# Kernel optimization log

Hardware: AMD Instinct MI355X
Metric: run time of the kernel (lower is better)

Reference implementation:

```python
import jax, jax.numpy as jnp
import numpy as np

D = 1024        # d_model
H = 16          # query heads
HKV = 4         # kv heads (GQA)
HD = D // H     # head dim = 64
MAX_T = 1024
EPS = 1e-6
CAP = 50.0      # logit softcap


def _rope_cache(max_t, hd):
    inv = 1.0 / (10000.0 ** (np.arange(0, hd, 2, dtype=np.float32) / hd))  # (hd/2,)
    t = np.arange(max_t, dtype=np.float32)
    f = np.outer(t, inv)                                                   # (max_t, hd/2)
    return jnp.asarray(np.cos(f)), jnp.asarray(np.sin(f))


def setup_inputs() -> dict:
    key = jax.random.key(0)
    ks = jax.random.split(key, 5)
    x = jax.random.normal(ks[0], (2, 64, 256, D), jnp.float32)  # (B,T,S,D)
    wq = jax.random.normal(ks[1], (D, H * HD), jnp.float32) * 0.02
    wk = jax.random.normal(ks[2], (D, HKV * HD), jnp.float32) * 0.02
    wv = jax.random.normal(ks[3], (D, HKV * HD), jnp.float32) * 0.02
    wo = jax.random.normal(ks[4], (H * HD, D), jnp.float32) * 0.02
    q_scale = jnp.ones((HD,), jnp.float32)  # QKNorm learnable gains
    k_scale = jnp.ones((HD,), jnp.float32)
    rope_cos, rope_sin = _rope_cache(MAX_T, HD)
    return {"x": x, "wq": wq, "wk": wk, "wv": wv, "wo": wo,
            "q_scale": q_scale, "k_scale": k_scale,
            "rope_cos": rope_cos, "rope_sin": rope_sin}


def _rmsnorm(v, scale):
    return v * jax.lax.rsqrt(jnp.mean(v * v, axis=-1, keepdims=True) + EPS) * scale


def reference(x, wq, wk, wv, wo, q_scale, k_scale, rope_cos, rope_sin):
    B, T, S, Dm = x.shape
    # fold spatial positions into batch: each position attends causally over time
    xt = x.transpose(0, 2, 1, 3).reshape(B * S, T, Dm)          # (N,T,D)
    q = (xt @ wq).reshape(B * S, T, H, HD)
    k = (xt @ wk).reshape(B * S, T, HKV, HD)
    v = (xt @ wv).reshape(B * S, T, HKV, HD)
    # QK-norm (RMSNorm over head_dim) before RoPE
    q = _rmsnorm(q, q_scale)
    k = _rmsnorm(k, k_scale)
    # 1D RoPE over temporal positions (split-half convention)
    cos = rope_cos[:T][None, :, None, :]                        # (1,T,1,HD/2)
    sin = rope_sin[:T][None, :, None, :]

    def rot(u):
        u1, u2 = jnp.split(u, 2, axis=-1)
        return jnp.concatenate([u1 * cos - u2 * sin, u1 * sin + u2 * cos], axis=-1)

    q = rot(q)
    k = rot(k)
    # GQA: expand kv heads to match query heads
    rep = H // HKV
    k = jnp.repeat(k, rep, axis=2)
    v = jnp.repeat(v, rep, axis=2)
    scores = jnp.einsum('nthd,nshd->nhts', q, k) / np.float32(np.sqrt(HD))
    scores = CAP * jnp.tanh(scores / CAP)                        # logit softcap
    causal = jnp.tril(jnp.ones((T, T), bool))
    scores = jnp.where(causal, scores, jnp.float32(-1e30))
    a = jax.nn.softmax(scores, axis=-1)
    o = jnp.einsum('nhts,nshd->nthd', a, v).reshape(B * S, T, H * HD) @ wo
    return o.reshape(B, S, T, Dm).transpose(0, 2, 1, 3)          # (B,T,S,D)
```

## Files before the change

kernel.cpp:

```cpp
#include <hip/hip_runtime.h>
#include <hip/hip_bf16.h>

#define DM   1024
#define NHQ  16
#define NKVH 4
#define HDIM 64
#define TTT  64
#define SSS  256
#define NBB  2
#define MROWS 32768

using short8 = __attribute__((ext_vector_type(8))) short;
using short4v = __attribute__((ext_vector_type(4))) short;
using f32x4  = __attribute__((ext_vector_type(4))) float;

__device__ __forceinline__ short f2bf(float f) {
  union { __hip_bfloat16 h; short s; } u;
  u.h = __float2bfloat16(f);
  return u.s;
}

__device__ __forceinline__ f32x4 mfma16(short8 a, short8 b, f32x4 c) {
  return __builtin_amdgcn_mfma_f32_16x16x32_bf16(a, b, c, 0, 0, 0);
}

__device__ __forceinline__ void gload_lds16(const void* g, void* l) {
  __builtin_amdgcn_global_load_lds(
      (const __attribute__((address_space(1))) void*)g,
      (__attribute__((address_space(3))) void*)l, 16, 0, 0);
}

__global__ __launch_bounds__(256) void k_prep(const float* __restrict__ x,
                                              short* __restrict__ xb,
                                              const float* __restrict__ wq,
                                              const float* __restrict__ wk,
                                              const float* __restrict__ wv,
                                              const float* __restrict__ wo,
                                              short* __restrict__ wqkvT,
                                              short* __restrict__ woT) {
  __shared__ float tile[32][33];
  int bid = blockIdx.x;
  if (bid < 4096) {
    float4 v[8];
    #pragma unroll
    for (int i = 0; i < 8; ++i) {
      int r = bid * 8 + i;
      int n = r >> 6, t = r & 63;
      int b = n >> 8, s = n & 255;
      v[i] = ((const float4*)(x + ((size_t)((b * TTT + t) * SSS + s)) * DM))[threadIdx.x];
    }
    #pragma unroll
    for (int i = 0; i < 8; ++i) {
      int r = bid * 8 + i;
      short4 o;
      o.x = f2bf(v[i].x); o.y = f2bf(v[i].y); o.z = f2bf(v[i].z); o.w = f2bf(v[i].w);
      ((short4*)(xb + (size_t)r * DM))[threadIdx.x] = o;
    }
    return;
  }
  bid -= 4096;
  const float* w; short* wt; int cols;
  if (bid < 1024)      { w = wq; wt = wqkvT; cols = 1024; }
  else if (bid < 1280) { w = wk; wt = wqkvT + (size_t)1024 * 1024; cols = 256; bid -= 1024; }
  else if (bid < 1536) { w = wv; wt = wqkvT + (size_t)1280 * 1024; cols = 256; bid -= 1280; }
  else                 { w = wo; wt = woT; cols = 1024; bid -= 1536; }
  int ctiles = cols >> 5;
  int tj = bid % ctiles;
  int td = bid / ctiles;
  int lx = threadIdx.x & 31, ly = threadIdx.x >> 5;
  #pragma unroll
  for (int rr = 0; rr < 32; rr += 8)
    tile[rr + ly][lx] = w[(size_t)(td * 32 + rr + ly) * cols + tj * 32 + lx];
  __syncthreads();
  #pragma unroll
  for (int rr = 0; rr < 32; rr += 8)
    wt[(size_t)(tj * 32 + rr + ly) * 1024 + td * 32 + lx] = f2bf(tile[lx][rr + ly]);
}

#define TILE(RAK0, RAK1, RBK0, RBK1, NLB, CLB, G, IA, IB, VM)                  \
  {                                                                            \
    short8 a[4], b0[4], b1[4];                                                 \
    _Pragma("unroll") for (int n = 0; n < 4; ++n)                              \
        b0[n] = *(const short8*)(RBK0 + n * 1024);                             \
    _Pragma("unroll") for (int m = 0; m < 4; ++m)                              \
        a[m] = *(const short8*)(RAK0 + m * 1024);                              \
    if (IA) stA0(NLB, (G + 1) * 64);                                           \
    __builtin_amdgcn_s_barrier();                                              \
    asm volatile("s_waitcnt lgkmcnt(0)" ::: "memory");                         \
    __builtin_amdgcn_s_setprio(1);                                             \
    _Pragma("unroll") for (int m = 0; m < 4; ++m)                              \
      _Pragma("unroll") for (int n = 0; n < 4; ++n)                            \
          acc[m][n] = mfma16(a[m], b0[n], acc[m][n]);                          \
    __builtin_amdgcn_s_setprio(0);                                             \
    __builtin_amdgcn_s_barrier();                                              \
    _Pragma("unroll") for (int m = 0; m < 4; ++m)                              \
        a[m] = *(const short8*)(RAK0 + 4096 + m * 1024);                       \
    if (IA) stA1(NLB, (G + 1) * 64);                                           \
    __builtin_amdgcn_s_barrier();                                              \
    asm volatile("s_waitcnt lgkmcnt(0)" ::: "memory");                         \
    __builtin_amdgcn_s_setprio(1);                                             \
    _Pragma("unroll") for (int m = 0; m < 4; ++m)                              \
      _Pragma("unroll") for (int n = 0; n < 4; ++n)                            \
          acc[4 + m][n] = mfma16(a[m], b0[n], acc[4 + m][n]);                  \
    __builtin_amdgcn_s_setprio(0);                                             \
    __builtin_amdgcn_s_barrier();                                              \
    _Pragma("unroll") for (int n = 0; n < 4; ++n)                              \
        b1[n] = *(const short8*)(RBK1 + n * 1024);                             \
    _Pragma("unroll") for (int m = 0; m < 4; ++m)                              \
        a[m] = *(const short8*)(RAK1 + m * 1024);                              \
    __builtin_amdgcn_s_barrier();                                              \
    asm volatile("s_waitcnt lgkmcnt(0)" ::: "memory");                         \
    __builtin_amdgcn_s_setprio(1);                                             \
    _Pragma("unroll") for (int m = 0; m < 4; ++m)                              \
      _Pragma("unroll") for (int n = 0; n < 4; ++n)                            \
          acc[m][n] = mfma16(a[m], b1[n], acc[m][n]);                          \
    __builtin_amdgcn_s_setprio(0);                                             \
    __builtin_amdgcn_s_barrier();                                              \
    _Pragma("unroll") for (int m = 0; m < 4; ++m)                              \
        a[m] = *(const short8*)(RAK1 + 4096 + m * 1024);                       \
    if (IB) stB(CLB, (G + 2) * 64);                                            \
    __builtin_amdgcn_s_barrier();                                              \
    asm volatile("s_waitcnt lgkmcnt(0)" ::: "memory");                         \
    __builtin_amdgcn_s_setprio(1);                                             \
    _Pragma("unroll") for (int m = 0; m < 4; ++m)                              \
      _Pragma("unroll") for (int n = 0; n < 4; ++n)                            \
          acc[4 + m][n] = mfma16(a[m], b1[n], acc[4 + m][n]);                  \
    __builtin_amdgcn_s_setprio(0);                                             \
    if (VM == 4)      asm volatile("s_waitcnt vmcnt(4)" ::: "memory");         \
    else if (VM == 0) asm volatile("s_waitcnt vmcnt(0)" ::: "memory");         \
    __builtin_amdgcn_s_barrier();                                              \
  }

__device__ __forceinline__ void gemm256(const short* __restrict__ Ab,
                                        const short* __restrict__ Bb,
                                        short* __restrict__ sm,
                                        f32x4 (&acc)[8][4]) {
  const int tid = threadIdx.x, lane = tid & 63, wid = tid >> 6;
  const int wr = wid >> 2, wc = wid & 3;
  const int ln15 = lane & 15, lhi = lane >> 4;
  const int rsw = ln15 & 7;
  const int row_t = tid >> 3;
  const int sw = ((tid & 7) ^ (row_t & 7)) << 3;
  const short* pA0 = Ab + (size_t)row_t * 1024 + sw;
  const short* pA1 = pA0 + (size_t)64 * 1024;
  const short* pA2 = pA0 + (size_t)128 * 1024;
  const short* pA3 = pA0 + (size_t)192 * 1024;
  const short* pB0 = Bb + (size_t)row_t * 1024 + sw;
  const short* pB1 = pB0 + (size_t)64 * 1024;
  const short* pB2 = pB0 + (size_t)128 * 1024;
  const short* pB3 = pB0 + (size_t)192 * 1024;
  auto stA0 = [&](short* lb, int kt) {
    gload_lds16(pA0 + kt, lb + tid * 8);
    gload_lds16(pA1 + kt, lb + 4096 + tid * 8);
  };
  auto stA1 = [&](short* lb, int kt) {
    gload_lds16(pA2 + kt, lb + 8192 + tid * 8);
    gload_lds16(pA3 + kt, lb + 12288 + tid * 8);
  };
  auto stB = [&](short* lb, int kt) {
    gload_lds16(pB0 + kt, lb + 16384 + tid * 8);
    gload_lds16(pB1 + kt, lb + 20480 + tid * 8);
    gload_lds16(pB2 + kt, lb + 24576 + tid * 8);
    gload_lds16(pB3 + kt, lb + 28672 + tid * 8);
  };
  const int sk0 = (lhi ^ rsw) << 3;
  const int sk1 = ((4 + lhi) ^ rsw) << 3;
  const short* rA0k0 = sm + (wr * 128 + ln15) * 64 + sk0;
  const short* rA0k1 = sm + (wr * 128 + ln15) * 64 + sk1;
  const short* rB0k0 = sm + 16384 + (wc * 64 + ln15) * 64 + sk0;
  const short* rB0k1 = sm + 16384 + (wc * 64 + ln15) * 64 + sk1;
  const short* rA1k0 = rA0k0 + 32768;
  const short* rA1k1 = rA0k1 + 32768;
  const short* rB1k0 = rB0k0 + 32768;
  const short* rB1k1 = rB0k1 + 32768;
  short* buf0 = sm;
  short* buf1 = sm + 32768;
  stA0(buf0, 0); stA1(buf0, 0); stB(buf0, 0);
  stA0(buf1, 64); stA1(buf1, 64); stB(buf1, 64);
  asm volatile("s_waitcnt vmcnt(8)" ::: "memory");
  __builtin_amdgcn_s_barrier();
  TILE(rA0k0, rA0k1, rB0k0, rB0k1, buf1, buf0, 0, 0, 1, 4)
  TILE(rA1k0, rA1k1, rB1k0, rB1k1, buf0, buf1, 1, 1, 1, 4)
  for (int gg = 1; gg < 7; ++gg) {
    const int g0 = gg * 2;
    TILE(rA0k0, rA0k1, rB0k0, rB0k1, buf1, buf0, g0, 1, 1, 4)
    TILE(rA1k0, rA1k1, rB1k0, rB1k1, buf0, buf1, g0 + 1, 1, 1, 4)
  }
  TILE(rA0k0, rA0k1, rB0k0, rB0k1, buf1, buf0, 14, 1, 0, 0)
  TILE(rA1k0, rA1k1, rB1k0, rB1k1, buf0, buf1, 15, 0, 0, -1)
}

__global__ __launch_bounds__(512) void k_qkv(
    const short* __restrict__ xb, const short* __restrict__ wt,
    const float* __restrict__ qscale, const float* __restrict__ kscale,
    const float* __restrict__ rcos, const float* __restrict__ rsin,
    short* __restrict__ qb, short* __restrict__ kb, short* __restrict__ vb) {
  __shared__ __align__(16) short sm[65536];
  const int bid = blockIdx.x;
  const int swz = (bid & 7) * 96 + (bid >> 3);
  const int tn = swz % 6, tm = swz / 6;
  f32x4 acc[8][4] = {};
  gemm256(xb + (size_t)tm * 256 * 1024, wt + (size_t)tn * 256 * 1024, sm, acc);

  const int tid = threadIdx.x, lane = tid & 63, wid = tid >> 6;
  const int wr = wid >> 2, wc = wid & 3;
  const int ln15 = lane & 15, lhi = lane >> 4;
  short* ot = sm;
  if (tn < 5) {
    const float* scale = (tn < 4) ? qscale : kscale;
    float sc[4];
    #pragma unroll
    for (int n = 0; n < 4; ++n) sc[n] = scale[n * 16 + ln15];
    #pragma unroll
    for (int m = 0; m < 8; ++m) {
      #pragma unroll
      for (int j = 0; j < 4; ++j) {
        float ss = 0.f;
        #pragma unroll
        for (int n = 0; n < 4; ++n) { float v = acc[m][n][j]; ss += v * v; }
        #pragma unroll
        for (int off = 8; off; off >>= 1) ss += __shfl_xor(ss, off, 64);
        float rms = rsqrtf(ss * (1.f / 64.f) + 1e-6f);
        int rl = wr * 128 + m * 16 + lhi * 4 + j;
        int t = (tm * 256 + rl) & 63;
        #pragma unroll
        for (int n = 0; n < 2; ++n) {
          int i = n * 16 + ln15;
          float cs = rcos[t * 32 + i], sn = rsin[t * 32 + i];
          float v1 = acc[m][n][j] * rms * sc[n];
          float v2 = acc[m][n + 2][j] * rms * sc[n + 2];
          ot[rl * 256 + wc * 64 + i]      = f2bf(v1 * cs - v2 * sn);
          ot[rl * 256 + wc * 64 + i + 32] = f2bf(v1 * sn + v2 * cs);
        }
      }
    }
  } else {
    #pragma unroll
    for (int m = 0; m < 8; ++m)
      #pragma unroll
      for (int n = 0; n < 4; ++n)
        #pragma unroll
        for (int j = 0; j < 4; ++j) {
          int rl = wr * 128 + m * 16 + lhi * 4 + j;
          ot[rl * 256 + wc * 64 + n * 16 + ln15] = f2bf(acc[m][n][j]);
        }
  }
  __syncthreads();
  {
    int row = tid >> 1, half = tid & 1;
    int r = tm * 256 + row;
    const uint4* src = (const uint4*)(ot + row * 256 + half * 128);
    short* dst;
    if (tn < 4)       dst = qb + (size_t)r * 1024 + tn * 256 + half * 128;
    else if (tn == 4) dst = kb + (size_t)r * 256 + half * 128;
    else              dst = vb + (size_t)r * 256 + half * 128;
    uint4* d4 = (uint4*)dst;
    #pragma unroll
    for (int i = 0; i < 16; ++i) d4[i] = src[i];
  }
}

__global__ __launch_bounds__(512) void k_attn(const short* __restrict__ qb,
                                              const short* __restrict__ kb,
                                              const short* __restrict__ vb,
                                              short* __restrict__ ob) {
  __shared__ __align__(16) short Vt[256 * 72];
  __shared__ __align__(16) short Ps[8][64 * 72];
  const int n = blockIdx.x;
  const int tid = threadIdx.x, lane = tid & 63, wid = tid >> 6;
  const int ln15 = lane & 15, lhi = lane >> 4;
  {
    const short* vrow = vb + ((size_t)(n * 64 + lane)) * 256;
    #pragma unroll
    for (int i = 0; i < 4; ++i) {
      int d = wid * 32 + i * 8;
      short8 vv = *(const short8*)(vrow + d);
      #pragma unroll
      for (int e = 0; e < 8; ++e) Vt[(d + e) * 72 + lane] = vv[e];
    }
  }
  short8 aq[2][4][2];
  #pragma unroll
  for (int hh = 0; hh < 2; ++hh)
    #pragma unroll
    for (int nn = 0; nn < 4; ++nn)
      #pragma unroll
      for (int kk = 0; kk < 2; ++kk)
        aq[hh][nn][kk] = *(const short8*)(qb + ((size_t)(n * 64 + nn * 16 + ln15)) * 1024
                                             + (wid + hh * 8) * 64 + kk * 32 + lhi * 8);
  __syncthreads();
  short* Pt = &Ps[wid][0];
  #pragma unroll
  for (int hh = 0; hh < 2; ++hh) {
    const int h = wid + hh * 8;
    const int kvh = h >> 2;
    short8 bk[4][2];
    #pragma unroll
    for (int m = 0; m < 4; ++m)
      #pragma unroll
      for (int kk = 0; kk < 2; ++kk)
        bk[m][kk] = *(const short8*)(kb + ((size_t)(n * 64 + m * 16 + ln15)) * 256
                                        + kvh * 64 + kk * 32 + lhi * 8);
    f32x4 sa[4][4] = {};
    __builtin_amdgcn_s_setprio(1);
    #pragma unroll
    for (int kk = 0; kk < 2; ++kk)
      #pragma unroll
      for (int m = 0; m < 4; ++m)
        #pragma unroll
        for (int nn = 0; nn < 4; ++nn)
          sa[m][nn] = mfma16(bk[m][kk], aq[hh][nn][kk], sa[m][nn]);
    __builtin_amdgcn_s_setprio(0);
    #pragma unroll
    for (int m = 0; m < 4; ++m)
      #pragma unroll
      for (int nn = 0; nn < 4; ++nn)
        #pragma unroll
        for (int j = 0; j < 4; ++j) {
          float e2 = __expf(sa[m][nn][j] * 0.005f);
          float cap = 50.f * (e2 - 1.f) * __builtin_amdgcn_rcpf(e2 + 1.f);
          int scur = m * 16 + lhi * 4 + j, tcur = nn * 16 + ln15;
          sa[m][nn][j] = (scur <= tcur) ? cap : -1e30f;
        }
    float inv[4];
    #pragma unroll
    for (int nn = 0; nn < 4; ++nn) {
      float mx = -3e38f;
      #pragma unroll
      for (int m = 0; m < 4; ++m)
        #pragma unroll
        for (int j = 0; j < 4; ++j) mx = fmaxf(mx, sa[m][nn][j]);
      mx = fmaxf(mx, __shfl_xor(mx, 16, 64));
      mx = fmaxf(mx, __shfl_xor(mx, 32, 64));
      float sum = 0.f;
      #pragma unroll
      for (int m = 0; m < 4; ++m)
        #pragma unroll
        for (int j = 0; j < 4; ++j) {
          float e = __expf(sa[m][nn][j] - mx);
          sa[m][nn][j] = e; sum += e;
        }
      sum += __shfl_xor(sum, 16, 64);
      sum += __shfl_xor(sum, 32, 64);
      inv[nn] = __builtin_amdgcn_rcpf(sum);
    }
    #pragma unroll
    for (int nn = 0; nn < 4; ++nn)
      #pragma unroll
      for (int m = 0; m < 4; ++m) {
        short4v w;
        #pragma unroll
        for (int j = 0; j < 4; ++j) w[j] = f2bf(sa[m][nn][j] * inv[nn]);
        *(short4v*)(Pt + (nn * 16 + ln15) * 72 + m * 16 + lhi * 4) = w;
      }
    short8 ap[4][2], bv[4][2];
    #pragma unroll
    for (int m = 0; m < 4; ++m)
      #pragma unroll
      for (int kk = 0; kk < 2; ++kk)
        ap[m][kk] = *(const short8*)(Pt + (m * 16 + ln15) * 72 + kk * 32 + lhi * 8);
    #pragma unroll
    for (int nn = 0; nn < 4; ++nn)
      #pragma unroll
      for (int kk = 0; kk < 2; ++kk)
        bv[nn][kk] = *(const short8*)(&Vt[(kvh * 64 + nn * 16 + ln15) * 72 + kk * 32 + lhi * 8]);
    f32x4 oa[4][4] = {};
    __builtin_amdgcn_s_setprio(1);
    #pragma unroll
    for (int kk = 0; kk < 2; ++kk)
      #pragma unroll
      for (int m = 0; m < 4; ++m)
        #pragma unroll
        for (int nn = 0; nn < 4; ++nn)
          oa[m][nn] = mfma16(ap[m][kk], bv[nn][kk], oa[m][nn]);
    __builtin_amdgcn_s_setprio(0);
    #pragma unroll
    for (int m = 0; m < 4; ++m)
      #pragma unroll
      for (int nn = 0; nn < 4; ++nn)
        #pragma unroll
        for (int j = 0; j < 4; ++j)
          Pt[(m * 16 + lhi * 4 + j) * 72 + nn * 16 + ln15] = f2bf(oa[m][nn][j]);
    #pragma unroll
    for (int c = 0; c < 8; ++c)
      *(uint4*)(ob + ((size_t)(n * 64 + lane)) * 1024 + h * 64 + c * 8)
          = *(const uint4*)(Pt + lane * 72 + c * 8);
  }
}

__global__ __launch_bounds__(512) void k_out(const short* __restrict__ ab,
                                             const short* __restrict__ wt,
                                             float* __restrict__ out) {
  __shared__ __align__(16) short sm[65536];
  const int bid = blockIdx.x;
  const int swz = (bid & 7) * 64 + (bid >> 3);
  const int tn = swz & 3, tm = swz >> 2;
  f32x4 acc[8][4] = {};
  gemm256(ab + (size_t)tm * 256 * 1024, wt + (size_t)tn * 256 * 1024, sm, acc);

  const int tid = threadIdx.x, lane = tid & 63, wid = tid >> 6;
  const int wr = wid >> 2, wc = wid & 3;
  const int ln15 = lane & 15, lhi = lane >> 4;
  float* of = (float*)sm;
  #pragma unroll
  for (int ch = 0; ch < 2; ++ch) {
    if (wr == ch) {
      #pragma unroll
      for (int m = 0; m < 8; ++m)
        #pragma unroll
        for (int n = 0; n < 4; ++n)
          #pragma unroll
          for (int j = 0; j < 4; ++j)
            of[(m * 16 + lhi * 4 + j) * 256 + wc * 64 + n * 16 + ln15] = acc[m][n][j];
    }
    __syncthreads();
    {
      int row = tid >> 2, q4 = tid & 3;
      int r = tm * 256 + ch * 128 + row;
      int nseq = r >> 6, t = r & 63;
      int b = nseq >> 8, s = nseq & 255;
      float* dst = out + ((size_t)((b * TTT + t) * SSS + s)) * DM + tn * 256 + q4 * 64;
      const float4* src = (const float4*)(of + row * 256 + q4 * 64);
      float4* d4 = (float4*)dst;
      #pragma unroll
      for (int i = 0; i < 16; ++i) d4[i] = src[i];
    }
    __syncthreads();
  }
}

extern "C" void kernel_launch(void* const* d_in, const int* in_sizes, int n_in,
                              void* d_out, int out_size, void* d_ws, size_t ws_size,
                              hipStream_t stream) {
  const float* x  = (const float*)d_in[0];
  const float* wq = (const float*)d_in[1];
  const float* wk = (const float*)d_in[2];
  const float* wv = (const float*)d_in[3];
  const float* wo = (const float*)d_in[4];
  const float* qs = (const float*)d_in[5];
  const float* ks = (const float*)d_in[6];
  const float* rc = (const float*)d_in[7];
  const float* rs = (const float*)d_in[8];
  float* out = (float*)d_out;
  char* ws = (char*)d_ws;

  short* xb    = (short*)(ws);
  short* wqkvT = (short*)(ws + 67108864);
  short* woT   = (short*)(ws + 70254592);
  short* qb    = (short*)(ws + 72351744);
  short* kb    = (short*)(ws + 139460608);
  short* vb    = (short*)(ws + 156237824);
  short* ob    = xb;

  k_prep<<<6656, 256, 0, stream>>>(x, xb, wq, wk, wv, wo, wqkvT, woT);
  k_qkv<<<768, 512, 0, stream>>>(xb, wqkvT, qs, ks, rc, rs, qb, kb, vb);
  k_attn<<<512, 512, 0, stream>>>(qb, kb, vb, ob);
  k_out<<<512, 512, 0, stream>>>(ob, woT, out);
}
```

Before: 323.0 us.

## Process two sequences per attention block with double-buffered V prefetch

Each attention block now handles two consecutive (batch*spatial) sequences instead of one, and the grid is halved. V rows for both sequences are loaded into registers up front, with the second sequence's V written to a second LDS buffer while the first is processed. This aims to hide global load latency and amortize block launch cost. The trade-off is more LDS per block and more register pressure, which may lower occupancy, and with 256 blocks some CUs may sit idle.

Measured after the change: 318.8 us (median of 2 runs). Within noise of the previous version (-1.3%).

```diff
diff --git a/kernel.cpp b/kernel.cpp
--- a/kernel.cpp
+++ b/kernel.cpp
@@ -264,127 +264,145 @@
                                               const short* __restrict__ kb,
                                               const short* __restrict__ vb,
                                               short* __restrict__ ob) {
-  __shared__ __align__(16) short Vt[256 * 72];
+  __shared__ __align__(16) short Vt[2][256 * 72];
   __shared__ __align__(16) short Ps[8][64 * 72];
-  const int n = blockIdx.x;
+  const int n0 = blockIdx.x * 2;
   const int tid = threadIdx.x, lane = tid & 63, wid = tid >> 6;
   const int ln15 = lane & 15, lhi = lane >> 4;
+  short8 vr0[4], vr1[4];
   {
-    const short* vrow = vb + ((size_t)(n * 64 + lane)) * 256;
-    #pragma unroll
-    for (int i = 0; i < 4; ++i) {
-      int d = wid * 32 + i * 8;
-      short8 vv = *(const short8*)(vrow + d);
-      #pragma unroll
-      for (int e = 0; e < 8; ++e) Vt[(d + e) * 72 + lane] = vv[e];
-    }
-  }
-  short8 aq[2][4][2];
+    const short* vrow0 = vb + ((size_t)(n0 * 64 + lane)) * 256;
+    const short* vrow1 = vrow0 + 64 * 256;
+    #pragma unroll
+    for (int i = 0; i < 4; ++i) vr1[i] = *(const short8*)(vrow1 + wid * 32 + i * 8);
+    #pragma unroll
+    for (int i = 0; i < 4; ++i) vr0[i] = *(const short8*)(vrow0 + wid * 32 + i * 8);
+  }
   #pragma unroll
-  for (int hh = 0; hh < 2; ++hh)
-    #pragma unroll
-    for (int nn = 0; nn < 4; ++nn)
-      #pragma unroll
-      for (int kk = 0; kk < 2; ++kk)
-        aq[hh][nn][kk] = *(const short8*)(qb + ((size_t)(n * 64 + nn * 16 + ln15)) * 1024
-                                             + (wid + hh * 8) * 64 + kk * 32 + lhi * 8);
-  __syncthreads();
+  for (int i = 0; i < 4; ++i) {
+    int d = wid * 32 + i * 8;
+    #pragma unroll
+    for (int e = 0; e < 8; ++e) Vt[0][(d + e) * 72 + lane] = vr0[i][e];
+  }
   short* Pt = &Ps[wid][0];
   #pragma unroll
-  for (int hh = 0; hh < 2; ++hh) {
-    const int h = wid + hh * 8;
-    const int kvh = h >> 2;
-    short8 bk[4][2];
-    #pragma unroll
-    for (int m = 0; m < 4; ++m)
+  for (int ss = 0; ss < 2; ++ss) {
+    const int n = n0 + ss;
+    if (ss == 1) {
+      #pragma unroll
+      for (int i = 0; i < 4; ++i) {
+        int d = wid * 32 + i * 8;
+        #pragma unroll
+        for (int e = 0; e < 8; ++e) Vt[1][(d + e) * 72 + lane] = vr1[i][e];
+      }
+    }
+    short8 aq[2][4][2];
+    #pragma unroll
+    for (int hh = 0; hh < 2; ++hh)
+      #pragma unroll
+      for (int nn = 0; nn < 4; ++nn)
+        #pragma unroll
+        for (int kk = 0; kk < 2; ++kk)
+          aq[hh][nn][kk] = *(const short8*)(qb + ((size_t)(n * 64 + nn * 16 + ln15)) * 1024
+                                               + (wid + hh * 8) * 64 + kk * 32 + lhi * 8);
+    __syncthreads();
+    const short* Vts = &Vt[ss][0];
+    #pragma unroll
+    for (int hh = 0; hh < 2; ++hh) {
+      const int h = wid + hh * 8;
+      const int kvh = h >> 2;
+      short8 bk[4][2];
+      #pragma unroll
+      for (int m = 0; m < 4; ++m)
+        #pragma unroll
+        for (int kk = 0; kk < 2; ++kk)
+          bk[m][kk] = *(const short8*)(kb + ((size_t)(n * 64 + m * 16 + ln15)) * 256
+                                          + kvh * 64 + kk * 32 + lhi * 8);
+      f32x4 sa[4][4] = {};
+      __builtin_amdgcn_s_setprio(1);
       #pragma unroll
       for (int kk = 0; kk < 2; ++kk)
-        bk[m][kk] = *(const short8*)(kb + ((size_t)(n * 64 + m * 16 + ln15)) * 256
-                                        + kvh * 64 + kk * 32 + lhi * 8);
-    f32x4 sa[4][4] = {};
-    __builtin_amdgcn_s_setprio(1);
-    #pragma unroll
-    for (int kk = 0; kk < 2; ++kk)
+        #pragma unroll
+        for (int m = 0; m < 4; ++m)
+          #pragma unroll
+          for (int nn = 0; nn < 4; ++nn)
+            sa[m][nn] = mfma16(bk[m][kk], aq[hh][nn][kk], sa[m][nn]);
+      __builtin_amdgcn_s_setprio(0);
       #pragma unroll
       for (int m = 0; m < 4; ++m)
         #pragma unroll
         for (int nn = 0; nn < 4; ++nn)
-          sa[m][nn] = mfma16(bk[m][kk], aq[hh][nn][kk], sa[m][nn]);
-    __builtin_amdgcn_s_setprio(0);
-    #pragma unroll
-    for (int m = 0; m < 4; ++m)
+          #pragma unroll
+          for (int j = 0; j < 4; ++j) {
+            float e2 = __expf(sa[m][nn][j] * 0.005f);
+            float cap = 50.f * (e2 - 1.f) * __builtin_amdgcn_rcpf(e2 + 1.f);
+            int scur = m * 16 + lhi * 4 + j, tcur = nn * 16 + ln15;
+            sa[m][nn][j] = (scur <= tcur) ? cap : -1e30f;
+          }
+      float inv[4];
+      #pragma unroll
+      for (int nn = 0; nn < 4; ++nn) {
+        float mx = -3e38f;
+        #pragma unroll
+        for (int m = 0; m < 4; ++m)
+          #pragma unroll
+          for (int j = 0; j < 4; ++j) mx = fmaxf(mx, sa[m][nn][j]);
+        mx = fmaxf(mx, __shfl_xor(mx, 16, 64));
+        mx = fmaxf(mx, __shfl_xor(mx, 32, 64));
+        float sum = 0.f;
+        #pragma unroll
+        for (int m = 0; m < 4; ++m)
+          #pragma unroll
+          for (int j = 0; j < 4; ++j) {
+            float e = __expf(sa[m][nn][j] - mx);
+            sa[m][nn][j] = e; sum += e;
+          }
+        sum += __shfl_xor(sum, 16, 64);
+        sum += __shfl_xor(sum, 32, 64);
+        inv[nn] = __builtin_amdgcn_rcpf(sum);
+      }
       #pragma unroll
       for (int nn = 0; nn < 4; ++nn)
         #pragma unroll
-        for (int j = 0; j < 4; ++j) {
-          float e2 = __expf(sa[m][nn][j] * 0.005f);
-          float cap = 50.f * (e2 - 1.f) * __builtin_amdgcn_rcpf(e2 + 1.f);
-          int scur = m * 16 + lhi * 4 + j, tcur = nn * 16 + ln15;
-          sa[m][nn][j] = (scur <= tcur) ? cap : -1e30f;
+        for (int m = 0; m < 4; ++m) {
+          short4v w;
+          #pragma unroll
+          for (int j = 0; j < 4; ++j) w[j] = f2bf(sa[m][nn][j] * inv[nn]);
+          *(short4v*)(Pt + (nn * 16 + ln15) * 72 + m * 16 + lhi * 4) = w;
         }
-    float inv[4];
-    #pragma unroll
-    for (int nn = 0; nn < 4; ++nn) {
-      float mx = -3e38f;
+      short8 ap[4][2], bv[4][2];
       #pragma unroll
       for (int m = 0; m < 4; ++m)
         #pragma unroll
-        for (int j = 0; j < 4; ++j) mx = fmaxf(mx, sa[m][nn][j]);
-      mx = fmaxf(mx, __shfl_xor(mx, 16, 64));
-      mx = fmaxf(mx, __shfl_xor(mx, 32, 64));
-      float sum = 0.f;
+        for (int kk = 0; kk < 2; ++kk)
+          ap[m][kk] = *(const short8*)(Pt + (m * 16 + ln15) * 72 + kk * 32 + lhi * 8);
+      #pragma unroll
+      for (int nn = 0; nn < 4; ++nn)
+        #pragma unroll
+        for (int kk = 0; kk < 2; ++kk)
+          bv[nn][kk] = *(const short8*)(Vts + (kvh * 64 + nn * 16 + ln15) * 72 + kk * 32 + lhi * 8);
+      f32x4 oa[4][4] = {};
+      __builtin_amdgcn_s_setprio(1);
+      #pragma unroll
+      for (int kk = 0; kk < 2; ++kk)
+        #pragma unroll
+        for (int m = 0; m < 4; ++m)
+          #pragma unroll
+          for (int nn = 0; nn < 4; ++nn)
+            oa[m][nn] = mfma16(ap[m][kk], bv[nn][kk], oa[m][nn]);
+      __builtin_amdgcn_s_setprio(0);
       #pragma unroll
       for (int m = 0; m < 4; ++m)
         #pragma unroll
-        for (int j = 0; j < 4; ++j) {
-          float e = __expf(sa[m][nn][j] - mx);
-          sa[m][nn][j] = e; sum += e;
-        }
-      sum += __shfl_xor(sum, 16, 64);
-      sum += __shfl_xor(sum, 32, 64);
-      inv[nn] = __builtin_amdgcn_rcpf(sum);
-    }
-    #pragma unroll
-    for (int nn = 0; nn < 4; ++nn)
-      #pragma unroll
-      for (int m = 0; m < 4; ++m) {
-        short4v w;
-        #pragma unroll
-        for (int j = 0; j < 4; ++j) w[j] = f2bf(sa[m][nn][j] * inv[nn]);
-        *(short4v*)(Pt + (nn * 16 + ln15) * 72 + m * 16 + lhi * 4) = w;
-      }
-    short8 ap[4][2], bv[4][2];
-    #pragma unroll
-    for (int m = 0; m < 4; ++m)
-      #pragma unroll
-      for (int kk = 0; kk < 2; ++kk)
-        ap[m][kk] = *(const short8*)(Pt + (m * 16 + ln15) * 72 + kk * 32 + lhi * 8);
-    #pragma unroll
-    for (int nn = 0; nn < 4; ++nn)
-      #pragma unroll
-      for (int kk = 0; kk < 2; ++kk)
-        bv[nn][kk] = *(const short8*)(&Vt[(kvh * 64 + nn * 16 + ln15) * 72 + kk * 32 + lhi * 8]);
-    f32x4 oa[4][4] = {};
-    __builtin_amdgcn_s_setprio(1);
-    #pragma unroll
-    for (int kk = 0; kk < 2; ++kk)
-      #pragma unroll
-      for (int m = 0; m < 4; ++m)
-        #pragma unroll
         for (int nn = 0; nn < 4; ++nn)
-          oa[m][nn] = mfma16(ap[m][kk], bv[nn][kk], oa[m][nn]);
-    __builtin_amdgcn_s_setprio(0);
-    #pragma unroll
-    for (int m = 0; m < 4; ++m)
-      #pragma unroll
-      for (int nn = 0; nn < 4; ++nn)
-        #pragma unroll
-        for (int j = 0; j < 4; ++j)
-          Pt[(m * 16 + lhi * 4 + j) * 72 + nn * 16 + ln15] = f2bf(oa[m][nn][j]);
-    #pragma unroll
-    for (int c = 0; c < 8; ++c)
-      *(uint4*)(ob + ((size_t)(n * 64 + lane)) * 1024 + h * 64 + c * 8)
-          = *(const uint4*)(Pt + lane * 72 + c * 8);
+          #pragma unroll
+          for (int j = 0; j < 4; ++j)
+            Pt[(m * 16 + lhi * 4 + j) * 72 + nn * 16 + ln15] = f2bf(oa[m][nn][j]);
+      #pragma unroll
+      for (int c = 0; c < 8; ++c)
+        *(uint4*)(ob + ((size_t)(n * 64 + lane)) * 1024 + h * 64 + c * 8)
+            = *(const uint4*)(Pt + lane * 72 + c * 8);
+    }
   }
 }
 
@@ -454,6 +472,6 @@
 
   k_prep<<<6656, 256, 0, stream>>>(x, xb, wq, wk, wv, wo, wqkvT, woT);
   k_qkv<<<768, 512, 0, stream>>>(xb, wqkvT, qs, ks, rc, rs, qb, kb, vb);
-  k_attn<<<512, 512, 0, stream>>>(qb, kb, vb, ob);
+  k_attn<<<256, 512, 0, stream>>>(qb, kb, vb, ob);
   k_out<<<512, 512, 0, stream>>>(ob, woT, out);
 }
```
